# Kernel optimization log

Hardware: AMD Instinct MI355X
Metric: run time of the kernel (lower is better)

Reference implementation:

```python
import jax, jax.numpy as jnp
import numpy as np

B, S, D, H = 16, 512, 256, 8
DH = D // H


def setup_inputs() -> dict:
    key = jax.random.key(0)
    ks = jax.random.split(key, 10)
    w_scale = 1.0 / np.sqrt(D)
    query = jax.random.normal(ks[0], (B, S, D), dtype=jnp.float32)
    key_t = jax.random.normal(ks[1], (B, S, D), dtype=jnp.float32)
    value = jax.random.normal(ks[2], (B, S, D), dtype=jnp.float32)
    rel = jax.random.uniform(ks[3], (B, S, S), dtype=jnp.float32)
    timestamp = jax.random.uniform(ks[4], (B, S, S), dtype=jnp.float32) * 100.0
    # causal mask: True = masked (future), as used by masked_fill in the torch code
    mask = jnp.broadcast_to(jnp.triu(jnp.ones((S, S), dtype=bool), k=1), (B, S, S))
    l1 = jnp.array(0.3, dtype=jnp.float32)
    l2 = jnp.array(0.4, dtype=jnp.float32)
    Wq = jax.random.normal(ks[5], (D, D), dtype=jnp.float32) * w_scale
    Wk = jax.random.normal(ks[6], (D, D), dtype=jnp.float32) * w_scale
    Wv = jax.random.normal(ks[7], (D, D), dtype=jnp.float32) * w_scale
    bq = jnp.zeros((D,), dtype=jnp.float32)
    bk = jnp.zeros((D,), dtype=jnp.float32)
    bv = jnp.zeros((D,), dtype=jnp.float32)
    return {"query": query, "key": key_t, "value": value, "rel": rel,
            "timestamp": timestamp, "mask": mask, "l1": l1, "l2": l2,
            "Wq": Wq, "bq": bq, "Wk": Wk, "bk": bk, "Wv": Wv, "bv": bv}


def _proj(x, W, b):
    # nn.Linear: x @ W.T + b, then split heads -> [B, H, S, DH]
    return (x @ W.T + b).reshape(B, S, H, DH).transpose(0, 2, 1, 3)


def reference(query, key, value, rel, timestamp, mask, l1, l2,
              Wq, bq, Wk, bk, Wv, bv):
    q = _proj(query, Wq, bq)
    k = _proj(key, Wk, bk)
    v = _proj(value, Wv, bv)
    m = mask[:, None]                      # [B,1,S,S], broadcasts over heads
    # relative-coefficient attention: keep rel where mask True, -10000 elsewhere
    relf = rel[:, None] * m.astype(jnp.float32)
    rel_attn = jax.nn.softmax(jnp.where(relf == 0, jnp.float32(-10000.0), relf), axis=-1)
    # scaled dot-product scores
    scores = jnp.einsum('bhqd,bhkd->bhqk', q, k) / jnp.sqrt(jnp.float32(DH))
    scores = jnp.where(m, jnp.float32(-1e9), scores)
    # time-decay attention
    ts = jnp.exp(-jnp.abs(timestamp))[:, None]
    ts = jnp.where(m, -jnp.inf, ts)
    prob_attn = jax.nn.softmax(scores, axis=-1)
    time_attn = jax.nn.softmax(ts, axis=-1)
    prob_attn = (1 - l2) * prob_attn + l2 * time_attn
    prob_attn = (1 - l1) * prob_attn + l1 * rel_attn
    out = jnp.einsum('bhqk,bhkd->bhqd', prob_attn, v)
    out = out.transpose(0, 2, 1, 3).reshape(B, S, D)
    return out, prob_attn
```

## Files before the change

kernel.cpp:

```cpp
#include <hip/hip_runtime.h>
#include <hip/hip_bf16.h>

static constexpr int cB  = 16;
static constexpr int cS  = 512;
static constexpr int cD  = 256;
static constexpr int cH  = 8;
static constexpr int cDH = 32;
static constexpr size_t cNE = (size_t)cB * cS * cD;
static constexpr size_t cWN = (size_t)cD * cD;

typedef __attribute__((ext_vector_type(8))) short short8v;
typedef __attribute__((ext_vector_type(4))) short short4v;
typedef __attribute__((ext_vector_type(4))) float f32x4;

__device__ __forceinline__ short bfbits(float x) {
    __hip_bfloat16 h = __float2bfloat16(x);
    short s; __builtin_memcpy(&s, &h, 2); return s;
}
__device__ __forceinline__ float bff(short s) {
    __hip_bfloat16 h; __builtin_memcpy(&h, &s, 2); return __bfloat162float(h);
}

__global__ __launch_bounds__(256) void wsplit_kernel(
    const float* __restrict__ Wq, const float* __restrict__ Wk,
    const float* __restrict__ Wv, short* __restrict__ Wsp)
{
    const int z = blockIdx.y;
    const float* W = (z == 0) ? Wq : (z == 1) ? Wk : Wv;
    short* hi = Wsp + (size_t)z * 2 * cWN;
    short* lo = hi + cWN;
    const int i = (blockIdx.x * 256 + threadIdx.x) * 4;
    float4 v = *(const float4*)(W + i);
    float va[4] = {v.x, v.y, v.z, v.w};
    short4v h, l;
#pragma unroll
    for (int j = 0; j < 4; j++) {
        short hb = bfbits(va[j]);
        h[j] = hb;
        l[j] = bfbits(va[j] - bff(hb));
    }
    *(short4v*)(hi + i) = h;
    *(short4v*)(lo + i) = l;
}

__global__ __launch_bounds__(256) void prep_kernel(
    const float* __restrict__ q_in, const float* __restrict__ k_in,
    const float* __restrict__ v_in, const short* __restrict__ Wsp,
    const float* __restrict__ bq, const float* __restrict__ bk,
    const float* __restrict__ bv,
    const float* __restrict__ rel, const float* __restrict__ ts,
    const float* __restrict__ l1p, const float* __restrict__ l2p,
    float* __restrict__ ws, short* __restrict__ Evb)
{
    const int bid = blockIdx.x;
    const int tid = threadIdx.x;
    const int w    = tid >> 6;
    const int lane = tid & 63;

    if (bid < 768) {
        const int z  = bid >> 8;
        const int bx = bid & 255;
        const float* X    = (z == 0) ? q_in : (z == 1) ? k_in : v_in;
        const float* bias = (z == 0) ? bq   : (z == 1) ? bk   : bv;
        const short* Whi = Wsp + (size_t)z * 2 * cWN;
        const short* Wlo = Whi + cWN;
        short* HI  = (short*)ws + (size_t)z * 2 * cNE;
        short* LO  = HI + cNE;
        short* VTb = (short*)(ws + 2 * cNE);

        const int n16  = lane & 15;
        const int quad = lane >> 4;
        const int i0 = bx * 32 + 16 * (w & 1);
        const int j0 = 128 * (w >> 1);

        const float* xrow = X + (size_t)(i0 + n16) * cD + quad * 8;
        short8v a_hi[8], a_lo[8];
#pragma unroll
        for (int c = 0; c < 8; c++) {
            float xa[8];
            *(float4*)&xa[0] = *(const float4*)(xrow + c * 32);
            *(float4*)&xa[4] = *(const float4*)(xrow + c * 32 + 4);
#pragma unroll
            for (int j = 0; j < 8; j++) {
                short hb = bfbits(xa[j]);
                a_hi[c][j] = hb;
                a_lo[c][j] = bfbits(xa[j] - bff(hb));
            }
        }

#pragma unroll
        for (int t = 0; t < 8; t++) {
            const int jb = j0 + t * 16;
            const size_t wbase = (size_t)(jb + n16) * cD + quad * 8;
            f32x4 acc = (f32x4){0.f, 0.f, 0.f, 0.f};
#pragma unroll
            for (int c = 0; c < 8; c++) {
                short8v b_hi = *(const short8v*)(Whi + wbase + c * 32);
                short8v b_lo = *(const short8v*)(Wlo + wbase + c * 32);
                acc = __builtin_amdgcn_mfma_f32_16x16x32_bf16(a_hi[c], b_hi, acc, 0, 0, 0);
                acc = __builtin_amdgcn_mfma_f32_16x16x32_bf16(a_hi[c], b_lo, acc, 0, 0, 0);
                acc = __builtin_amdgcn_mfma_f32_16x16x32_bf16(a_lo[c], b_hi, acc, 0, 0, 0);
            }
            const int jg = jb + n16;
            const float bv_ = bias[jg];
            const int h_ = jg >> 5, dh = jg & 31;
            if (z == 2) {
#pragma unroll
                for (int r = 0; r < 4; r++) {
                    int gi = i0 + quad * 4 + r;
                    int b_ = gi >> 9, s_ = gi & 511;
                    VTb[(((size_t)(b_ * cH + h_)) * cDH + dh) * cS + s_] =
                        bfbits(acc[r] + bv_);
                }
            } else {
#pragma unroll
                for (int r = 0; r < 4; r++) {
                    int gi = i0 + quad * 4 + r;
                    int b_ = gi >> 9, s_ = gi & 511;
                    size_t idx = (((size_t)(b_ * cH + h_)) * cS + s_) * cDH + dh;
                    float v = acc[r] + bv_;
                    short hb2 = bfbits(v);
                    HI[idx] = hb2;
                    LO[idx] = bfbits(v - bff(hb2));
                }
            }
        }
    } else {
        const int row = (bid - 768) * 4 + w;
        const int q = row & 511;
        const float* tr = ts  + (size_t)row * cS;
        const float* rr = rel + (size_t)row * cS;
        const float l1 = l1p[0], l2 = l2p[0];
        const float Bc = (1.f - l1) * l2;
        const float Cc = l1;

        float tv[8], rv[8];
        float tmax = -1e30f, rmax = -1e30f;
#pragma unroll
        for (int j = 0; j < 8; j++) {
            int k = lane + 64 * j;
            float tl_ = (k <= q) ? tr[k] : 0.f;
            float r   = (k >  q) ? rr[k] : 0.f;
            tv[j] = (k <= q) ? __expf(-fabsf(tl_)) : -1e30f;
            rv[j] = (k > q && r != 0.f) ? r : -10000.f;
            tmax = fmaxf(tmax, tv[j]);
            rmax = fmaxf(rmax, rv[j]);
        }
#pragma unroll
        for (int m = 1; m < 64; m <<= 1) {
            tmax = fmaxf(tmax, __shfl_xor(tmax, m, 64));
            rmax = fmaxf(rmax, __shfl_xor(rmax, m, 64));
        }
        float te[8], re[8];
        float tsum = 0.f, rsum = 0.f;
#pragma unroll
        for (int j = 0; j < 8; j++) {
            te[j] = (tv[j] > -1e29f) ? __expf(tv[j] - tmax) : 0.f;
            re[j] = __expf(rv[j] - rmax);
            tsum += te[j]; rsum += re[j];
        }
#pragma unroll
        for (int m = 1; m < 64; m <<= 1) {
            tsum += __shfl_xor(tsum, m, 64);
            rsum += __shfl_xor(rsum, m, 64);
        }
        const float ti = Bc / tsum, ri = Cc / rsum;
#pragma unroll
        for (int j = 0; j < 8; j++) {
            int k = lane + 64 * j;
            Evb[(size_t)row * cS + k] = bfbits(te[j] * ti + re[j] * ri);
        }
    }
}

__global__ __launch_bounds__(256, 4) void attn2_kernel(
    const float* __restrict__ ws, const short* __restrict__ Evb,
    const float* __restrict__ l1p, const float* __restrict__ l2p,
    float* __restrict__ out, float* __restrict__ prob)
{
    constexpr int PS = 536;
    __shared__ short Pl[32 * PS];
    __shared__ float redM[2][32];
    __shared__ float redS[2][32];

    const int tid  = threadIdx.x;
    const int w    = tid >> 6;
    const int lane = tid & 63;
    const int n16  = lane & 15;
    const int quad = lane >> 4;

    const int flat = blockIdx.y * gridDim.x + blockIdx.x;
    const int xcd  = flat & 7;
    const int slot = flat >> 3;
    const int b  = xcd + 8 * (slot >> 7);
    const int h  = (slot >> 4) & 7;
    const int qt = slot & 15;
    const size_t bh = (size_t)b * cH + h;
    const int q0 = qt * 32;

    const short* Qhi = (const short*)ws;
    const short* Qlo = Qhi + cNE;
    const short* Khi = Qhi + 2 * cNE;
    const short* Klo = Qhi + 3 * cNE;
    const short* VTb = (const short*)(ws + 2 * cNE);

    const float l1 = l1p[0], l2 = l2p[0];
    const float Ac = (1.f - l1) * (1.f - l2);

    const int qhH = w & 1;
    const int kh2 = w >> 1;
    const int kbase = 256 * kh2;

    const int rowA = q0 + 16 * qhH + n16;
    const size_t qoff = (bh * cS + rowA) * cDH + quad * 8;
    short8v a_hi = *(const short8v*)(Qhi + qoff);
    short8v a_lo = *(const short8v*)(Qlo + qoff);

    const int tl = (kbase <= q0 + 31) ? min(15, (q0 + 31 - kbase) >> 4) : -1;
    f32x4 acc[16];
#pragma unroll
    for (int t = 0; t < 16; t++) {
        acc[t] = (f32x4){0.f, 0.f, 0.f, 0.f};
        if (t <= tl) {
            const size_t koff = (bh * cS + kbase + 16 * t + n16) * cDH + quad * 8;
            short8v b_hi = *(const short8v*)(Khi + koff);
            short8v b_lo = *(const short8v*)(Klo + koff);
            acc[t] = __builtin_amdgcn_mfma_f32_16x16x32_bf16(a_hi, b_hi, acc[t], 0, 0, 0);
            acc[t] = __builtin_amdgcn_mfma_f32_16x16x32_bf16(a_hi, b_lo, acc[t], 0, 0, 0);
            acc[t] = __builtin_amdgcn_mfma_f32_16x16x32_bf16(a_lo, b_hi, acc[t], 0, 0, 0);
        }
    }

    const float scale = 0.17677669529663687f;
    const int rowDl = 16 * qhH + quad * 4;
    float Mx0 = -1e30f, Mx1 = -1e30f, Mx2 = -1e30f, Mx3 = -1e30f;
#pragma unroll
    for (int t = 0; t < 16; t++) {
        const int kg = kbase + 16 * t + n16;
        const int rg = q0 + rowDl;
        float s0 = (kg <= rg + 0) ? acc[t][0] * scale : -1e30f;
        float s1 = (kg <= rg + 1) ? acc[t][1] * scale : -1e30f;
        float s2 = (kg <= rg + 2) ? acc[t][2] * scale : -1e30f;
        float s3 = (kg <= rg + 3) ? acc[t][3] * scale : -1e30f;
        acc[t][0] = s0; acc[t][1] = s1; acc[t][2] = s2; acc[t][3] = s3;
        Mx0 = fmaxf(Mx0, s0); Mx1 = fmaxf(Mx1, s1);
        Mx2 = fmaxf(Mx2, s2); Mx3 = fmaxf(Mx3, s3);
    }
#pragma unroll
    for (int m = 1; m < 16; m <<= 1) {
        Mx0 = fmaxf(Mx0, __shfl_xor(Mx0, m, 64));
        Mx1 = fmaxf(Mx1, __shfl_xor(Mx1, m, 64));
        Mx2 = fmaxf(Mx2, __shfl_xor(Mx2, m, 64));
        Mx3 = fmaxf(Mx3, __shfl_xor(Mx3, m, 64));
    }
    if (n16 == 0) {
        redM[kh2][rowDl + 0] = Mx0; redM[kh2][rowDl + 1] = Mx1;
        redM[kh2][rowDl + 2] = Mx2; redM[kh2][rowDl + 3] = Mx3;
    }
    __syncthreads();
    float Mg0 = fmaxf(redM[0][rowDl + 0], redM[1][rowDl + 0]);
    float Mg1 = fmaxf(redM[0][rowDl + 1], redM[1][rowDl + 1]);
    float Mg2 = fmaxf(redM[0][rowDl + 2], redM[1][rowDl + 2]);
    float Mg3 = fmaxf(redM[0][rowDl + 3], redM[1][rowDl + 3]);

    float S0 = 0.f, S1 = 0.f, S2 = 0.f, S3 = 0.f;
#pragma unroll
    for (int t = 0; t < 16; t++) {
        float e0 = __expf(acc[t][0] - Mg0);
        float e1 = __expf(acc[t][1] - Mg1);
        float e2 = __expf(acc[t][2] - Mg2);
        float e3 = __expf(acc[t][3] - Mg3);
        acc[t][0] = e0; acc[t][1] = e1; acc[t][2] = e2; acc[t][3] = e3;
        S0 += e0; S1 += e1; S2 += e2; S3 += e3;
    }
#pragma unroll
    for (int m = 1; m < 16; m <<= 1) {
        S0 += __shfl_xor(S0, m, 64); S1 += __shfl_xor(S1, m, 64);
        S2 += __shfl_xor(S2, m, 64); S3 += __shfl_xor(S3, m, 64);
    }
    if (n16 == 0) {
        redS[kh2][rowDl + 0] = S0; redS[kh2][rowDl + 1] = S1;
        redS[kh2][rowDl + 2] = S2; redS[kh2][rowDl + 3] = S3;
    }
    __syncthreads();
    const float i0 = Ac / (redS[0][rowDl + 0] + redS[1][rowDl + 0]);
    const float i1 = Ac / (redS[0][rowDl + 1] + redS[1][rowDl + 1]);
    const float i2 = Ac / (redS[0][rowDl + 2] + redS[1][rowDl + 2]);
    const float i3 = Ac / (redS[0][rowDl + 3] + redS[1][rowDl + 3]);

#pragma unroll
    for (int t = 0; t < 16; t++) {
        const int col = kbase + 16 * t + n16;
        Pl[(rowDl + 0) * PS + col] = bfbits(acc[t][0] * i0);
        Pl[(rowDl + 1) * PS + col] = bfbits(acc[t][1] * i1);
        Pl[(rowDl + 2) * PS + col] = bfbits(acc[t][2] * i2);
        Pl[(rowDl + 3) * PS + col] = bfbits(acc[t][3] * i3);
    }
    __syncthreads();

#pragma unroll
    for (int it = 0; it < 16; it++) {
        const int idx = it * 256 + tid;
        const int r = idx >> 7;
        const int c0 = (idx & 127) * 4;
        short* pp = &Pl[r * PS + c0];
        short4v pv = *(short4v*)pp;
        const short4v ev = *(const short4v*)(Evb + ((size_t)(b * cS + q0 + r)) * cS + c0);
        f32x4 o;
#pragma unroll
        for (int j = 0; j < 4; j++) o[j] = bff(pv[j]) + bff(ev[j]);
        __builtin_nontemporal_store(o, (f32x4*)(prob + (bh * cS + q0 + r) * cS + c0));
#pragma unroll
        for (int j = 0; j < 4; j++) pv[j] = bfbits(o[j]);
        *(short4v*)pp = pv;
    }
    __syncthreads();

    const int dhT = w & 1, qT = w >> 1;
    const int dhA = 16 * dhT + n16;
    const short* vtrow = VTb + (bh * cDH + dhA) * cS;
    f32x4 oacc = (f32x4){0.f, 0.f, 0.f, 0.f};
#pragma unroll
    for (int k0 = 0; k0 < cS; k0 += 32) {
        short8v av = *(const short8v*)(vtrow + k0 + quad * 8);
        short8v bv = *(short8v*)&Pl[(16 * qT + n16) * PS + k0 + quad * 8];
        oacc = __builtin_amdgcn_mfma_f32_16x16x32_bf16(av, bv, oacc, 0, 0, 0);
    }
    const int qg = q0 + 16 * qT + n16;
    const int dhD = 16 * dhT + quad * 4;
    float* op = out + ((size_t)b * cS + qg) * cD + h * cDH + dhD;
    __builtin_nontemporal_store(oacc, (f32x4*)op);
}

extern "C" void kernel_launch(void* const* d_in, const int* in_sizes, int n_in,
                              void* d_out, int out_size, void* d_ws, size_t ws_size,
                              hipStream_t stream) {
    const float* query = (const float*)d_in[0];
    const float* key   = (const float*)d_in[1];
    const float* value = (const float*)d_in[2];
    const float* rel   = (const float*)d_in[3];
    const float* tsp   = (const float*)d_in[4];
    const float* l1 = (const float*)d_in[6];
    const float* l2 = (const float*)d_in[7];
    const float* Wq = (const float*)d_in[8];
    const float* bq = (const float*)d_in[9];
    const float* Wk = (const float*)d_in[10];
    const float* bk = (const float*)d_in[11];
    const float* Wv = (const float*)d_in[12];
    const float* bv = (const float*)d_in[13];

    float* ws   = (float*)d_ws;
    short* Evb  = (short*)(ws + 3 * cNE);
    short* Wsp  = Evb + (size_t)cB * cS * cS;
    float* out  = (float*)d_out;
    float* prob = out + cNE;

    wsplit_kernel<<<dim3(64, 3), 256, 0, stream>>>(Wq, Wk, Wv, Wsp);
    prep_kernel<<<dim3(2816), 256, 0, stream>>>(query, key, value, Wsp,
                                                bq, bk, bv, rel, tsp,
                                                l1, l2, ws, Evb);
    attn2_kernel<<<dim3(16, 128), 256, 0, stream>>>(ws, Evb, l1, l2, out, prob);
}
```

Before: 283.2 us.

## Shrink attention query tile to 16 rows and split keys across four waves

The attention kernel now handles 16 query rows per block instead of 32. Each of the four waves covers a 128-key slice, and the cross-wave max and sum reductions become four-way. The grid doubles, LDS per block halves, and the launch bound asks for 6 blocks per CU to raise occupancy and shorten the tail. In exchange, only two of four waves do the PV matmul, and K/V reads are repeated by twice as many blocks.

```diff
diff --git a/kernel.cpp b/kernel.cpp
--- a/kernel.cpp
+++ b/kernel.cpp
@@ -173,15 +173,15 @@
     }
 }
 
-__global__ __launch_bounds__(256, 4) void attn2_kernel(
+__global__ __launch_bounds__(256, 6) void attn16_kernel(
     const float* __restrict__ ws, const short* __restrict__ Evb,
     const float* __restrict__ l1p, const float* __restrict__ l2p,
     float* __restrict__ out, float* __restrict__ prob)
 {
     constexpr int PS = 536;
-    __shared__ short Pl[32 * PS];
-    __shared__ float redM[2][32];
-    __shared__ float redS[2][32];
+    __shared__ short Pl[16 * PS];
+    __shared__ float redM[4][16];
+    __shared__ float redS[4][16];
 
     const int tid  = threadIdx.x;
     const int w    = tid >> 6;
@@ -192,11 +192,11 @@
     const int flat = blockIdx.y * gridDim.x + blockIdx.x;
     const int xcd  = flat & 7;
     const int slot = flat >> 3;
-    const int b  = xcd + 8 * (slot >> 7);
-    const int h  = (slot >> 4) & 7;
-    const int qt = slot & 15;
+    const int b  = xcd + 8 * (slot >> 8);
+    const int h  = (slot >> 5) & 7;
+    const int qt = slot & 31;
     const size_t bh = (size_t)b * cH + h;
-    const int q0 = qt * 32;
+    const int q0 = qt * 16;
 
     const short* Qhi = (const short*)ws;
     const short* Qlo = Qhi + cNE;
@@ -207,19 +207,17 @@
     const float l1 = l1p[0], l2 = l2p[0];
     const float Ac = (1.f - l1) * (1.f - l2);
 
-    const int qhH = w & 1;
-    const int kh2 = w >> 1;
-    const int kbase = 256 * kh2;
-
-    const int rowA = q0 + 16 * qhH + n16;
+    const int kbase = 128 * w;
+
+    const int rowA = q0 + n16;
     const size_t qoff = (bh * cS + rowA) * cDH + quad * 8;
     short8v a_hi = *(const short8v*)(Qhi + qoff);
     short8v a_lo = *(const short8v*)(Qlo + qoff);
 
-    const int tl = (kbase <= q0 + 31) ? min(15, (q0 + 31 - kbase) >> 4) : -1;
-    f32x4 acc[16];
-#pragma unroll
-    for (int t = 0; t < 16; t++) {
+    const int tl = (kbase <= q0 + 15) ? min(7, (q0 + 15 - kbase) >> 4) : -1;
+    f32x4 acc[8];
+#pragma unroll
+    for (int t = 0; t < 8; t++) {
         acc[t] = (f32x4){0.f, 0.f, 0.f, 0.f};
         if (t <= tl) {
             const size_t koff = (bh * cS + kbase + 16 * t + n16) * cDH + quad * 8;
@@ -232,10 +230,10 @@
     }
 
     const float scale = 0.17677669529663687f;
-    const int rowDl = 16 * qhH + quad * 4;
+    const int rowDl = quad * 4;
     float Mx0 = -1e30f, Mx1 = -1e30f, Mx2 = -1e30f, Mx3 = -1e30f;
 #pragma unroll
-    for (int t = 0; t < 16; t++) {
+    for (int t = 0; t < 8; t++) {
         const int kg = kbase + 16 * t + n16;
         const int rg = q0 + rowDl;
         float s0 = (kg <= rg + 0) ? acc[t][0] * scale : -1e30f;
@@ -254,18 +252,22 @@
         Mx3 = fmaxf(Mx3, __shfl_xor(Mx3, m, 64));
     }
     if (n16 == 0) {
-        redM[kh2][rowDl + 0] = Mx0; redM[kh2][rowDl + 1] = Mx1;
-        redM[kh2][rowDl + 2] = Mx2; redM[kh2][rowDl + 3] = Mx3;
+        redM[w][rowDl + 0] = Mx0; redM[w][rowDl + 1] = Mx1;
+        redM[w][rowDl + 2] = Mx2; redM[w][rowDl + 3] = Mx3;
     }
     __syncthreads();
-    float Mg0 = fmaxf(redM[0][rowDl + 0], redM[1][rowDl + 0]);
-    float Mg1 = fmaxf(redM[0][rowDl + 1], redM[1][rowDl + 1]);
-    float Mg2 = fmaxf(redM[0][rowDl + 2], redM[1][rowDl + 2]);
-    float Mg3 = fmaxf(redM[0][rowDl + 3], redM[1][rowDl + 3]);
+    float Mg0 = fmaxf(fmaxf(redM[0][rowDl + 0], redM[1][rowDl + 0]),
+                      fmaxf(redM[2][rowDl + 0], redM[3][rowDl + 0]));
+    float Mg1 = fmaxf(fmaxf(redM[0][rowDl + 1], redM[1][rowDl + 1]),
+                      fmaxf(redM[2][rowDl + 1], redM[3][rowDl + 1]));
+    float Mg2 = fmaxf(fmaxf(redM[0][rowDl + 2], redM[1][rowDl + 2]),
+                      fmaxf(redM[2][rowDl + 2], redM[3][rowDl + 2]));
+    float Mg3 = fmaxf(fmaxf(redM[0][rowDl + 3], redM[1][rowDl + 3]),
+                      fmaxf(redM[2][rowDl + 3], redM[3][rowDl + 3]));
 
     float S0 = 0.f, S1 = 0.f, S2 = 0.f, S3 = 0.f;
 #pragma unroll
-    for (int t = 0; t < 16; t++) {
+    for (int t = 0; t < 8; t++) {
         float e0 = __expf(acc[t][0] - Mg0);
         float e1 = __expf(acc[t][1] - Mg1);
         float e2 = __expf(acc[t][2] - Mg2);
@@ -279,17 +281,21 @@
         S2 += __shfl_xor(S2, m, 64); S3 += __shfl_xor(S3, m, 64);
     }
     if (n16 == 0) {
-        redS[kh2][rowDl + 0] = S0; redS[kh2][rowDl + 1] = S1;
-        redS[kh2][rowDl + 2] = S2; redS[kh2][rowDl + 3] = S3;
+        redS[w][rowDl + 0] = S0; redS[w][rowDl + 1] = S1;
+        redS[w][rowDl + 2] = S2; redS[w][rowDl + 3] = S3;
     }
     __syncthreads();
-    const float i0 = Ac / (redS[0][rowDl + 0] + redS[1][rowDl + 0]);
-    const float i1 = Ac / (redS[0][rowDl + 1] + redS[1][rowDl + 1]);
-    const float i2 = Ac / (redS[0][rowDl + 2] + redS[1][rowDl + 2]);
-    const float i3 = Ac / (redS[0][rowDl + 3] + redS[1][rowDl + 3]);
-
-#pragma unroll
-    for (int t = 0; t < 16; t++) {
+    const float i0 = Ac / (redS[0][rowDl + 0] + redS[1][rowDl + 0] +
+                           redS[2][rowDl + 0] + redS[3][rowDl + 0]);
+    const float i1 = Ac / (redS[0][rowDl + 1] + redS[1][rowDl + 1] +
+                           redS[2][rowDl + 1] + redS[3][rowDl + 1]);
+    const float i2 = Ac / (redS[0][rowDl + 2] + redS[1][rowDl + 2] +
+                           redS[2][rowDl + 2] + redS[3][rowDl + 2]);
+    const float i3 = Ac / (redS[0][rowDl + 3] + redS[1][rowDl + 3] +
+                           redS[2][rowDl + 3] + redS[3][rowDl + 3]);
+
+#pragma unroll
+    for (int t = 0; t < 8; t++) {
         const int col = kbase + 16 * t + n16;
         Pl[(rowDl + 0) * PS + col] = bfbits(acc[t][0] * i0);
         Pl[(rowDl + 1) * PS + col] = bfbits(acc[t][1] * i1);
@@ -299,7 +305,7 @@
     __syncthreads();
 
 #pragma unroll
-    for (int it = 0; it < 16; it++) {
+    for (int it = 0; it < 8; it++) {
         const int idx = it * 256 + tid;
         const int r = idx >> 7;
         const int c0 = (idx & 127) * 4;
@@ -316,20 +322,21 @@
     }
     __syncthreads();
 
-    const int dhT = w & 1, qT = w >> 1;
-    const int dhA = 16 * dhT + n16;
-    const short* vtrow = VTb + (bh * cDH + dhA) * cS;
-    f32x4 oacc = (f32x4){0.f, 0.f, 0.f, 0.f};
-#pragma unroll
-    for (int k0 = 0; k0 < cS; k0 += 32) {
-        short8v av = *(const short8v*)(vtrow + k0 + quad * 8);
-        short8v bv = *(short8v*)&Pl[(16 * qT + n16) * PS + k0 + quad * 8];
-        oacc = __builtin_amdgcn_mfma_f32_16x16x32_bf16(av, bv, oacc, 0, 0, 0);
-    }
-    const int qg = q0 + 16 * qT + n16;
-    const int dhD = 16 * dhT + quad * 4;
-    float* op = out + ((size_t)b * cS + qg) * cD + h * cDH + dhD;
-    __builtin_nontemporal_store(oacc, (f32x4*)op);
+    if (w < 2) {
+        const int dhA = 16 * w + n16;
+        const short* vtrow = VTb + (bh * cDH + dhA) * cS;
+        f32x4 oacc = (f32x4){0.f, 0.f, 0.f, 0.f};
+#pragma unroll
+        for (int k0 = 0; k0 < cS; k0 += 32) {
+            short8v av = *(const short8v*)(vtrow + k0 + quad * 8);
+            short8v bv = *(short8v*)&Pl[n16 * PS + k0 + quad * 8];
+            oacc = __builtin_amdgcn_mfma_f32_16x16x32_bf16(av, bv, oacc, 0, 0, 0);
+        }
+        const int qg = q0 + n16;
+        const int dhD = 16 * w + quad * 4;
+        float* op = out + ((size_t)b * cS + qg) * cD + h * cDH + dhD;
+        __builtin_nontemporal_store(oacc, (f32x4*)op);
+    }
 }
 
 extern "C" void kernel_launch(void* const* d_in, const int* in_sizes, int n_in,
@@ -359,5 +366,5 @@
     prep_kernel<<<dim3(2816), 256, 0, stream>>>(query, key, value, Wsp,
                                                 bq, bk, bv, rel, tsp,
                                                 l1, l2, ws, Evb);
-    attn2_kernel<<<dim3(16, 128), 256, 0, stream>>>(ws, Evb, l1, l2, out, prob);
-}
+    attn16_kernel<<<dim3(32, 128), 256, 0, stream>>>(ws, Evb, l1, l2, out, prob);
+}
```

New measurement: 281.4 us. No clear change (-0.6%).
